# Performance work log

Measured on AMD Instinct MI355X. Metric: run time of the kernel, lower is better.

Reference implementation:

```python
import jax, jax.numpy as jnp
import numpy as np

SEQ, B, N, H, OUT, K, L = 32, 1024, 19, 128, 1, 2, 2


def setup_inputs() -> dict:
    key = jax.random.key(0)
    ks = jax.random.split(key, 16)
    s = lambda i, shape, scale=1.0: (jax.random.normal(ks[i], shape, jnp.float32) * scale)
    return {
        "inputs": s(0, (SEQ, B, N, OUT)),
        "initial_hidden_state": s(1, (L, B, N * H)),
        "support": s(2, (N, N)) * (1.0 / np.sqrt(N)),
        "W_gate0": s(3, (3 * (OUT + H), 2 * H)) * 0.05,
        "b_gate0": s(4, (2 * H,)) * 0.05,
        "W_cand0": s(5, (3 * (OUT + H), H)) * 0.05,
        "b_cand0": s(6, (H,)) * 0.05,
        "W_gate1": s(7, (3 * (H + H), 2 * H)) * 0.05,
        "b_gate1": s(8, (2 * H,)) * 0.05,
        "W_cand1": s(9, (3 * (H + H), H)) * 0.05,
        "b_cand1": s(10, (H,)) * 0.05,
        "W_proj": s(11, (H, OUT)) * 0.05,
        "b_proj": s(12, (OUT,)) * 0.05,
    }


def reference(inputs, initial_hidden_state, support, W_gate0, b_gate0, W_cand0,
              b_cand0, W_gate1, b_gate1, W_cand1, b_cand1, W_proj, b_proj):
    seq_len, batch = inputs.shape[0], inputs.shape[1]
    h0 = initial_hidden_state.reshape(L, batch, N, H)

    def gconv(x, W, b):
        # Chebyshev diffusion: x0, T1=S@x0, T2=2*S@T1-x0 (K=2, 1 support)
        x0 = x
        x1 = jnp.einsum('mn,bnf->bmf', support, x0)
        feats = [x0, x1]
        for _ in range(K - 1):
            x2 = 2.0 * jnp.einsum('mn,bnf->bmf', support, x1) - x0
            feats.append(x2)
            x0, x1 = x1, x2
        X = jnp.concatenate(feats, axis=-1)  # (B, N, F*num_matrices)
        return jnp.einsum('bnf,fo->bno', X, W) + b

    def cell(x_in, h, Wg, bg, Wc, bc):
        ru = jax.nn.sigmoid(gconv(jnp.concatenate([x_in, h], axis=-1), Wg, bg))
        r, u = jnp.split(ru, 2, axis=-1)
        c = jnp.tanh(gconv(jnp.concatenate([x_in, r * h], axis=-1), Wc, bc))
        return u * h + (1.0 - u) * c

    layer_params = [(W_gate0, b_gate0, W_cand0, b_cand0),
                    (W_gate1, b_gate1, W_cand1, b_cand1)]

    def step(carry, _):
        h, cur = carry
        new_h = []
        x = cur
        for i, (Wg, bg, Wc, bc) in enumerate(layer_params):
            x = cell(x, h[i], Wg, bg, Wc, bc)
            new_h.append(x)
        proj = jnp.einsum('bnh,ho->bno', x, W_proj) + b_proj  # (B, N, OUT)
        out_t = proj.reshape(batch, N * OUT)
        return (jnp.stack(new_h, axis=0), proj), out_t

    go = jnp.zeros((batch, N, OUT), inputs.dtype)
    (_, _), outputs = jax.lax.scan(step, (h0, go), None, length=seq_len)
    return outputs  # (seq_len, batch, N*OUT)
```

## Files before the change

kernel.cpp:

```cpp
#include <hip/hip_runtime.h>
#include <hip/hip_bf16.h>
#include <math.h>

#define SEQ   32
#define BATCH 1024
#define NN    19
#define HH    128
#define NB    4
#define MR    (NB*NN)
#define SAS   264
#define HS    132
#define UTS   72
#define NBLK  (BATCH/NB)
#define NT    512

#define OFF_G0 0
#define OFF_C0 122880
#define OFF_G1 184320
#define OFF_C1 380928
#define WTOT   479232

__device__ unsigned short g_wall[WTOT];
__device__ unsigned short g_tg[2048];

typedef __attribute__((ext_vector_type(8))) short  bf16x8;
typedef __attribute__((ext_vector_type(4))) float  f32x4;

__device__ __forceinline__ unsigned short f2bf(float v) {
    __hip_bfloat16 b = __float2bfloat16(v);
    return *reinterpret_cast<unsigned short*>(&b);
}
__device__ __forceinline__ float bf2f(unsigned short u) {
    unsigned int x = ((unsigned int)u) << 16;
    return __uint_as_float(x);
}
__device__ __forceinline__ float hload(const unsigned short* p) { return bf2f(*p); }
__device__ __forceinline__ float hload(const float* p)          { return *p; }
__device__ __forceinline__ void  hstore(unsigned short* p, float v) { *p = f2bf(v); }
__device__ __forceinline__ void  hstore(float* p, float v)          { *p = v; }

__global__ __launch_bounds__(256) void wconv_kernel(
    const float* __restrict__ W, int F, int O, int KP, int off)
{
    int idx = blockIdx.x*256 + threadIdx.x;
    int total = 3*O*KP;
    if (idx >= total) return;
    int j   = idx / (O*KP);
    int r   = idx - j*(O*KP);
    int col = r / KP;
    int k   = r - col*KP;
    float v = (k < F) ? W[(size_t)(j*F + k)*O + col] : 0.f;
    g_wall[off + idx] = f2bf(v);
}

__global__ __launch_bounds__(256) void tprime_kernel(const float* __restrict__ S)
{
    __shared__ float sS[NN*NN], sS2[NN*NN];
    int tid = threadIdx.x;
    for (int i = tid; i < NN*NN; i += 256) sS[i] = S[i];
    __syncthreads();
    for (int i = tid; i < NN*NN; i += 256) {
        int m = i/NN, n = i - m*NN;
        float a = 0.f;
        for (int k = 0; k < NN; ++k) a += sS[m*NN+k]*sS[k*NN+n];
        sS2[i] = a;
    }
    __syncthreads();
    for (int i = tid; i < 32*64; i += 256) {
        int m = i >> 6, k = i & 63;
        float v = 0.f;
        if (m < NN && k < 3*NN) {
            int j = k / NN, n = k - j*NN;
            float eye = (m == n) ? 1.f : 0.f;
            if (j == 0)      v = eye;
            else if (j == 1) v = sS[m*NN+n];
            else             v = 2.f*sS2[m*NN+n] - eye;
        }
        g_tg[i] = f2bf(v);
    }
}

#define LDS_BYTES 159664

template<int KS, int NTC, bool GATE, int XW, typename HT>
__device__ __forceinline__ void gconv_phase(
    const unsigned short* __restrict__ BT,
    const float* __restrict__ bias,
    HT* hL,
    unsigned short* sA,
    unsigned short* ub,
    unsigned short* UtW,
    int lane, int w)
{
    constexpr int OC = NTC*128;
    constexpr int KP = KS*32;
    const int r16 = lane & 15, quad = lane >> 4;
    const int sgo = w * (NTC*16);

    const unsigned short* wb[3][NTC];
    #pragma unroll
    for (int j = 0; j < 3; ++j)
        #pragma unroll
        for (int nt = 0; nt < NTC; ++nt)
            wb[j][nt] = BT + (size_t)(j*OC + sgo + nt*16 + r16)*KP + quad*8;

    f32x4 acc[3][5][NTC];
    #pragma unroll
    for (int j = 0; j < 3; ++j)
        #pragma unroll
        for (int mt = 0; mt < 5; ++mt)
            #pragma unroll
            for (int nt = 0; nt < NTC; ++nt) acc[j][mt][nt] = (f32x4)0.f;

    bf16x8 ring[2][3][NTC];
    #pragma unroll
    for (int j = 0; j < 3; ++j)
        #pragma unroll
        for (int nt = 0; nt < NTC; ++nt) {
            ring[0][j][nt] = *(const bf16x8*)(wb[j][nt]);
            if (KS > 1) ring[1][j][nt] = *(const bf16x8*)(wb[j][nt] + 32);
        }

    #pragma unroll
    for (int ks = 0; ks < KS; ++ks) {
        bf16x8 bcur[3][NTC];
        #pragma unroll
        for (int j = 0; j < 3; ++j)
            #pragma unroll
            for (int nt = 0; nt < NTC; ++nt) bcur[j][nt] = ring[ks & 1][j][nt];
        if (ks + 2 < KS) {
            #pragma unroll
            for (int j = 0; j < 3; ++j)
                #pragma unroll
                for (int nt = 0; nt < NTC; ++nt)
                    ring[ks & 1][j][nt] =
                        *(const bf16x8*)(wb[j][nt] + (ks + 2)*32);
        }
        #pragma unroll
        for (int mt = 0; mt < 5; ++mt) {
            bf16x8 af = *(const bf16x8*)&sA[(mt*16 + r16)*SAS + ks*32 + quad*8];
            #pragma unroll
            for (int j = 0; j < 3; ++j)
                #pragma unroll
                for (int nt = 0; nt < NTC; ++nt)
                    acc[j][mt][nt] = __builtin_amdgcn_mfma_f32_16x16x32_bf16(
                        af, bcur[j][nt], acc[j][mt][nt], 0, 0, 0);
        }
    }

    if (GATE) __syncthreads();

    float bv[NTC];
    #pragma unroll
    for (int nt = 0; nt < NTC; ++nt) bv[nt] = bias[sgo + nt*16 + r16];

    bf16x8 tp[2][2];
    #pragma unroll
    for (int mt2 = 0; mt2 < 2; ++mt2)
        #pragma unroll
        for (int kk = 0; kk < 2; ++kk)
            tp[mt2][kk] = *(const bf16x8*)&g_tg[(mt2*16 + r16)*64 + kk*32 + quad*8];

    for (int b = 0; b < NB; ++b) {
        #pragma unroll
        for (int j = 0; j < 3; ++j)
            #pragma unroll
            for (int mt = 0; mt < 5; ++mt)
                #pragma unroll
                for (int reg = 0; reg < 4; ++reg) {
                    int gm = mt*16 + quad*4 + reg;
                    int n  = gm - b*NN;
                    if (n >= 0 && n < NN) {
                        #pragma unroll
                        for (int nt = 0; nt < NTC; ++nt)
                            UtW[(nt*16 + r16)*UTS + j*NN + n] =
                                f2bf(acc[j][mt][nt][reg]);
                    }
                }
        f32x4 y[2][NTC];
        #pragma unroll
        for (int a = 0; a < 2; ++a)
            #pragma unroll
            for (int c = 0; c < NTC; ++c) y[a][c] = (f32x4)0.f;
        #pragma unroll
        for (int kk = 0; kk < 2; ++kk)
            #pragma unroll
            for (int nt = 0; nt < NTC; ++nt) {
                bf16x8 uf = *(const bf16x8*)&UtW[(nt*16 + r16)*UTS + kk*32 + quad*8];
                y[0][nt] = __builtin_amdgcn_mfma_f32_16x16x32_bf16(
                    tp[0][kk], uf, y[0][nt], 0, 0, 0);
                y[1][nt] = __builtin_amdgcn_mfma_f32_16x16x32_bf16(
                    tp[1][kk], uf, y[1][nt], 0, 0, 0);
            }
        #pragma unroll
        for (int mt2 = 0; mt2 < 2; ++mt2)
            #pragma unroll
            for (int nt = 0; nt < NTC; ++nt)
                #pragma unroll
                for (int reg = 0; reg < 4; ++reg) {
                    int m = mt2*16 + quad*4 + reg;
                    if (m < NN) {
                        int o = sgo + nt*16 + r16;
                        float v = y[mt2][nt][reg] + bv[nt];
                        int row = b*NN + m;
                        if (GATE) {
                            float sg_ = 1.f/(1.f + __expf(-v));
                            if (o < HH)
                                sA[row*SAS + XW + o] =
                                    f2bf(sg_ * hload(&hL[row*HS + o]));
                            else
                                ub[row*HS + (o-HH)] = f2bf(sg_);
                        } else {
                            float c  = 2.f/(1.f + __expf(-2.f*v)) - 1.f;
                            float u  = bf2f(ub[row*HS + o]);
                            float ho = hload(&hL[row*HS + o]);
                            hstore(&hL[row*HS + o], u*ho + (1.f - u)*c);
                        }
                    }
                }
    }
}

__global__ __launch_bounds__(NT, 2) void dcgru_persistent(
    const float* __restrict__ ihs,
    const float* __restrict__ bg0, const float* __restrict__ bc0,
    const float* __restrict__ bg1, const float* __restrict__ bc1,
    const float* __restrict__ Wp, const float* __restrict__ bp,
    float* __restrict__ out)
{
    extern __shared__ char smem[];
    unsigned short* h0    = (unsigned short*)smem;
    float*          h1    = (float*)(smem + 20064);
    unsigned short* sA    = (unsigned short*)(smem + 60192);
    unsigned short* ub    = (unsigned short*)(smem + 102432);
    unsigned short* Ut    = (unsigned short*)(smem + 122496);
    float*          xprev = (float*)(smem + 159360);

    const int tid  = threadIdx.x;
    const int lane = tid & 63;
    const int w    = tid >> 6;
    const int bb   = blockIdx.x * NB;
    unsigned short* UtW = Ut + w*32*UTS;

    const unsigned short* BTg0 = g_wall + OFF_G0;
    const unsigned short* BTc0 = g_wall + OFF_C0;
    const unsigned short* BTg1 = g_wall + OFF_G1;
    const unsigned short* BTc1 = g_wall + OFF_C1;

    for (int i = tid; i < MR*HH; i += NT) {
        int row = i >> 7, f = i & 127;
        h0[row*HS + f] = f2bf(ihs[(size_t)bb*2432 + i]);
        h1[row*HS + f] = ihs[(size_t)(BATCH + bb)*2432 + i];
    }
    for (int i = tid; i < MR; i += NT) xprev[i] = 0.f;
    for (int i = lane; i < 32*UTS; i += 64) UtW[i] = 0;

    const float wp0 = Wp[lane], wp1 = Wp[64 + lane], bpv = bp[0];
    __syncthreads();

    for (int t = 0; t < SEQ; ++t) {
        for (int idx = tid; idx < MR*160; idx += NT) {
            int row = idx/160, c = idx - row*160;
            unsigned short v;
            if (c == 0)       v = f2bf(xprev[row]);
            else if (c <= HH) v = h0[row*HS + (c-1)];
            else              v = 0;
            sA[row*SAS + c] = v;
        }
        __syncthreads();
        gconv_phase<5,2,true ,1>(BTg0, bg0, h0, sA, ub, UtW, lane, w);
        __syncthreads();
        gconv_phase<5,1,false,1>(BTc0, bc0, h0, sA, ub, UtW, lane, w);
        __syncthreads();

        for (int idx = tid; idx < MR*256; idx += NT) {
            int row = idx >> 8, c = idx & 255;
            sA[row*SAS + c] = (c < HH) ? h0[row*HS + c]
                                       : f2bf(h1[row*HS + (c-HH)]);
        }
        __syncthreads();
        gconv_phase<8,2,true ,HH>(BTg1, bg1, h1, sA, ub, UtW, lane, w);
        __syncthreads();
        gconv_phase<8,1,false,HH>(BTc1, bc1, h1, sA, ub, UtW, lane, w);
        __syncthreads();

        {
            int b  = w >> 1;
            int n0 = (w & 1) ? 10 : 0;
            int n1 = (w & 1) ? 19 : 10;
            for (int n = n0; n < n1; ++n) {
                int row = b*NN + n;
                float s = h1[row*HS + lane]*wp0 + h1[row*HS + 64 + lane]*wp1;
                #pragma unroll
                for (int off = 32; off; off >>= 1) s += __shfl_down(s, off, 64);
                if (lane == 0) {
                    float v = s + bpv;
                    out[((size_t)t*BATCH + bb + b)*NN + n] = v;
                    xprev[row] = v;
                }
            }
        }
        __syncthreads();
    }
}

extern "C" void kernel_launch(void* const* d_in, const int* in_sizes, int n_in,
                              void* d_out, int out_size, void* d_ws, size_t ws_size,
                              hipStream_t stream) {
    const float* ihs = (const float*)d_in[1];
    const float* S   = (const float*)d_in[2];
    const float* Wg0 = (const float*)d_in[3];
    const float* bg0 = (const float*)d_in[4];
    const float* Wc0 = (const float*)d_in[5];
    const float* bc0 = (const float*)d_in[6];
    const float* Wg1 = (const float*)d_in[7];
    const float* bg1 = (const float*)d_in[8];
    const float* Wc1 = (const float*)d_in[9];
    const float* bc1 = (const float*)d_in[10];
    const float* Wp  = (const float*)d_in[11];
    const float* bp  = (const float*)d_in[12];
    float* out = (float*)d_out;

    tprime_kernel<<<1, 256, 0, stream>>>(S);
    wconv_kernel<<<(3*256*160+255)/256, 256, 0, stream>>>(Wg0, 129, 256, 160, OFF_G0);
    wconv_kernel<<<(3*128*160+255)/256, 256, 0, stream>>>(Wc0, 129, 128, 160, OFF_C0);
    wconv_kernel<<<(3*256*256+255)/256, 256, 0, stream>>>(Wg1, 256, 256, 256, OFF_G1);
    wconv_kernel<<<(3*128*256+255)/256, 256, 0, stream>>>(Wc1, 256, 128, 256, OFF_C1);

    hipFuncSetAttribute((const void*)dcgru_persistent,
                        hipFuncAttributeMaxDynamicSharedMemorySize, LDS_BYTES);

    dcgru_persistent<<<NBLK, NT, LDS_BYTES, stream>>>(
        ihs, bg0, bc0, bg1, bc1, Wp, bp, out);
}
```

Measured before the change: 2.434 ms.

## Diffuse inputs before weight GEMM instead of diffusing per-weight outputs

Reorders the Chebyshev graph convolution so the support matrices (block-diagonal S and 2S²−I across the batch tile) are applied to the input features first via MFMA, and the three weight slices are then applied to X, S·X and T2·X in sequence. The old path used a per-batch U^T transpose through LDS and small diffusion MFMAs after the weight GEMM. The input column layout is also reordered (h first, x last) so that h0 can be copied with vectorised 16-byte loads. The cost is extra barriers between the three weight segments, ping-pong buffers A/B in LDS, and strided scalar LDS reads to build the diffusion operands.

```diff
diff --git a/kernel.cpp b/kernel.cpp
--- a/kernel.cpp
+++ b/kernel.cpp
@@ -9,8 +9,9 @@
 #define NB    4
 #define MR    (NB*NN)
 #define SAS   264
-#define HS    132
-#define UTS   72
+#define H0S   128
+#define H1S   132
+#define UBS   128
 #define NBLK  (BATCH/NB)
 #define NT    512
 
@@ -20,8 +21,16 @@
 #define OFF_C1 380928
 #define WTOT   479232
 
+#define OFF_H0 0
+#define OFF_H1 19456
+#define OFF_A  59584
+#define OFF_B  101824
+#define OFF_UB 144064
+#define OFF_XP 163520
+#define LDS_BYTES 163824
+
 __device__ unsigned short g_wall[WTOT];
-__device__ unsigned short g_tg[2048];
+__device__ unsigned short g_sb[2*80*96];
 
 typedef __attribute__((ext_vector_type(8))) short  bf16x8;
 typedef __attribute__((ext_vector_type(4))) float  f32x4;
@@ -40,7 +49,7 @@
 __device__ __forceinline__ void  hstore(float* p, float v)          { *p = v; }
 
 __global__ __launch_bounds__(256) void wconv_kernel(
-    const float* __restrict__ W, int F, int O, int KP, int off)
+    const float* __restrict__ W, int F, int O, int KP, int off, int l0)
 {
     int idx = blockIdx.x*256 + threadIdx.x;
     int total = 3*O*KP;
@@ -49,11 +58,14 @@
     int r   = idx - j*(O*KP);
     int col = r / KP;
     int k   = r - col*KP;
-    float v = (k < F) ? W[(size_t)(j*F + k)*O + col] : 0.f;
+    int src;
+    if (l0) src = (k < HH) ? k+1 : ((k == HH) ? 0 : -1);
+    else    src = (k < F) ? k : -1;
+    float v = (src >= 0) ? W[(size_t)(j*F + src)*O + col] : 0.f;
     g_wall[off + idx] = f2bf(v);
 }
 
-__global__ __launch_bounds__(256) void tprime_kernel(const float* __restrict__ S)
+__global__ __launch_bounds__(256) void sb_kernel(const float* __restrict__ S)
 {
     __shared__ float sS[NN*NN], sS2[NN*NN];
     int tid = threadIdx.x;
@@ -66,159 +78,178 @@
         sS2[i] = a;
     }
     __syncthreads();
-    for (int i = tid; i < 32*64; i += 256) {
-        int m = i >> 6, k = i & 63;
+    for (int i = tid; i < 2*80*96; i += 256) {
+        int mat = i / 7680;
+        int rr  = i - mat*7680;
+        int r   = rr / 96, k = rr - r*96;
         float v = 0.f;
-        if (m < NN && k < 3*NN) {
-            int j = k / NN, n = k - j*NN;
-            float eye = (m == n) ? 1.f : 0.f;
-            if (j == 0)      v = eye;
-            else if (j == 1) v = sS[m*NN+n];
-            else             v = 2.f*sS2[m*NN+n] - eye;
-        }
-        g_tg[i] = f2bf(v);
-    }
-}
-
-#define LDS_BYTES 159664
-
-template<int KS, int NTC, bool GATE, int XW, typename HT>
+        if (r < MR) {
+            int b = r / NN, m = r - b*NN;
+            int k0 = b*NN;
+            if (k >= k0 && k < k0 + NN) {
+                int n = k - k0;
+                v = (mat == 0) ? sS[m*NN+n]
+                               : (2.f*sS2[m*NN+n] - ((m==n)?1.f:0.f));
+            }
+        }
+        g_sb[i] = f2bf(v);
+    }
+}
+
+template<int KS, int NTC>
+__device__ __forceinline__ void load_wf(bf16x8 (&wf)[KS][NTC],
+    const unsigned short* __restrict__ Wj, int r16, int quad, int sgo)
+{
+    #pragma unroll
+    for (int ks = 0; ks < KS; ++ks)
+        #pragma unroll
+        for (int nt = 0; nt < NTC; ++nt)
+            wf[ks][nt] = *(const bf16x8*)(Wj +
+                (size_t)(sgo + nt*16 + r16)*(KS*32) + ks*32 + quad*8);
+}
+
+template<int KS, int NTC>
+__device__ __forceinline__ void mma_seg(f32x4 (&acc)[5][NTC],
+    const bf16x8 (&wf)[KS][NTC], const unsigned short* __restrict__ Ab,
+    int r16, int quad)
+{
+    #pragma unroll
+    for (int ks = 0; ks < KS; ++ks)
+        #pragma unroll
+        for (int mt = 0; mt < 5; ++mt) {
+            bf16x8 af = *(const bf16x8*)&Ab[(mt*16 + r16)*SAS + ks*32 + quad*8];
+            #pragma unroll
+            for (int nt = 0; nt < NTC; ++nt)
+                acc[mt][nt] = __builtin_amdgcn_mfma_f32_16x16x32_bf16(
+                    af, wf[ks][nt], acc[mt][nt], 0, 0, 0);
+        }
+}
+
+template<int KS, int NTC, bool GATE, int XW, int DCOLS, typename HT, int HSTR>
 __device__ __forceinline__ void gconv_phase(
-    const unsigned short* __restrict__ BT,
-    const float* __restrict__ bias,
-    HT* hL,
-    unsigned short* sA,
-    unsigned short* ub,
-    unsigned short* UtW,
+    const unsigned short* __restrict__ BT, const float* __restrict__ bias,
+    HT* __restrict__ hL,
+    unsigned short* __restrict__ Xb, unsigned short* __restrict__ Zb,
+    unsigned short* __restrict__ ub,
     int lane, int w)
 {
     constexpr int OC = NTC*128;
     constexpr int KP = KS*32;
     const int r16 = lane & 15, quad = lane >> 4;
-    const int sgo = w * (NTC*16);
-
-    const unsigned short* wb[3][NTC];
-    #pragma unroll
-    for (int j = 0; j < 3; ++j)
-        #pragma unroll
-        for (int nt = 0; nt < NTC; ++nt)
-            wb[j][nt] = BT + (size_t)(j*OC + sgo + nt*16 + r16)*KP + quad*8;
-
-    f32x4 acc[3][5][NTC];
-    #pragma unroll
-    for (int j = 0; j < 3; ++j)
+    const int sgo = w*(NTC*16);
+    const int c0  = w*32;
+    const bool dif = (c0 < DCOLS);
+
+    f32x4 z2a[5][2];
+    if (dif) {
+        constexpr int zmt[9] = {0,1,1,2,2,3,3,4,4};
+        constexpr int zks[9] = {0,0,1,0,1,1,2,1,2};
+        bf16x8 sb1[9], sb2[9], Bg[3][2];
+        #pragma unroll
+        for (int i = 0; i < 9; ++i) {
+            int o = (zmt[i]*16 + r16)*96 + zks[i]*32 + quad*8;
+            sb1[i] = *(const bf16x8*)&g_sb[o];
+            sb2[i] = *(const bf16x8*)&g_sb[7680 + o];
+        }
+        #pragma unroll
+        for (int kd = 0; kd < 3; ++kd)
+            #pragma unroll
+            for (int nt = 0; nt < 2; ++nt) {
+                bf16x8 v;
+                #pragma unroll
+                for (int e = 0; e < 8; ++e)
+                    v[e] = (short)Xb[(kd*32 + quad*8 + e)*SAS + c0 + nt*16 + r16];
+                Bg[kd][nt] = v;
+            }
+        f32x4 z1a[5][2];
         #pragma unroll
         for (int mt = 0; mt < 5; ++mt)
             #pragma unroll
-            for (int nt = 0; nt < NTC; ++nt) acc[j][mt][nt] = (f32x4)0.f;
-
-    bf16x8 ring[2][3][NTC];
-    #pragma unroll
-    for (int j = 0; j < 3; ++j)
-        #pragma unroll
-        for (int nt = 0; nt < NTC; ++nt) {
-            ring[0][j][nt] = *(const bf16x8*)(wb[j][nt]);
-            if (KS > 1) ring[1][j][nt] = *(const bf16x8*)(wb[j][nt] + 32);
-        }
-
-    #pragma unroll
-    for (int ks = 0; ks < KS; ++ks) {
-        bf16x8 bcur[3][NTC];
-        #pragma unroll
-        for (int j = 0; j < 3; ++j)
-            #pragma unroll
-            for (int nt = 0; nt < NTC; ++nt) bcur[j][nt] = ring[ks & 1][j][nt];
-        if (ks + 2 < KS) {
-            #pragma unroll
-            for (int j = 0; j < 3; ++j)
-                #pragma unroll
-                for (int nt = 0; nt < NTC; ++nt)
-                    ring[ks & 1][j][nt] =
-                        *(const bf16x8*)(wb[j][nt] + (ks + 2)*32);
-        }
-        #pragma unroll
-        for (int mt = 0; mt < 5; ++mt) {
-            bf16x8 af = *(const bf16x8*)&sA[(mt*16 + r16)*SAS + ks*32 + quad*8];
-            #pragma unroll
-            for (int j = 0; j < 3; ++j)
-                #pragma unroll
-                for (int nt = 0; nt < NTC; ++nt)
-                    acc[j][mt][nt] = __builtin_amdgcn_mfma_f32_16x16x32_bf16(
-                        af, bcur[j][nt], acc[j][mt][nt], 0, 0, 0);
-        }
-    }
-
-    if (GATE) __syncthreads();
+            for (int nt = 0; nt < 2; ++nt) {
+                z1a[mt][nt] = (f32x4)0.f; z2a[mt][nt] = (f32x4)0.f;
+            }
+        #pragma unroll
+        for (int i = 0; i < 9; ++i)
+            #pragma unroll
+            for (int nt = 0; nt < 2; ++nt) {
+                z1a[zmt[i]][nt] = __builtin_amdgcn_mfma_f32_16x16x32_bf16(
+                    sb1[i], Bg[zks[i]][nt], z1a[zmt[i]][nt], 0, 0, 0);
+                z2a[zmt[i]][nt] = __builtin_amdgcn_mfma_f32_16x16x32_bf16(
+                    sb2[i], Bg[zks[i]][nt], z2a[zmt[i]][nt], 0, 0, 0);
+            }
+        #pragma unroll
+        for (int mt = 0; mt < 5; ++mt)
+            #pragma unroll
+            for (int nt = 0; nt < 2; ++nt)
+                #pragma unroll
+                for (int reg = 0; reg < 4; ++reg)
+                    Zb[(mt*16 + quad*4 + reg)*SAS + c0 + nt*16 + r16] =
+                        f2bf(z1a[mt][nt][reg]);
+    }
+
+    f32x4 acc[5][NTC];
+    #pragma unroll
+    for (int mt = 0; mt < 5; ++mt)
+        #pragma unroll
+        for (int nt = 0; nt < NTC; ++nt) acc[mt][nt] = (f32x4)0.f;
+
+    {
+        bf16x8 wf[KS][NTC];
+        load_wf<KS,NTC>(wf, BT, r16, quad, sgo);
+        mma_seg<KS,NTC>(acc, wf, Xb, r16, quad);
+    }
+    __syncthreads();
+    if (dif) {
+        #pragma unroll
+        for (int mt = 0; mt < 5; ++mt)
+            #pragma unroll
+            for (int nt = 0; nt < 2; ++nt)
+                #pragma unroll
+                for (int reg = 0; reg < 4; ++reg)
+                    Xb[(mt*16 + quad*4 + reg)*SAS + c0 + nt*16 + r16] =
+                        f2bf(z2a[mt][nt][reg]);
+    }
+    {
+        bf16x8 wf[KS][NTC];
+        load_wf<KS,NTC>(wf, BT + (size_t)OC*KP, r16, quad, sgo);
+        mma_seg<KS,NTC>(acc, wf, Zb, r16, quad);
+    }
+    __syncthreads();
+    {
+        bf16x8 wf[KS][NTC];
+        load_wf<KS,NTC>(wf, BT + (size_t)2*OC*KP, r16, quad, sgo);
+        mma_seg<KS,NTC>(acc, wf, Xb, r16, quad);
+    }
 
     float bv[NTC];
     #pragma unroll
     for (int nt = 0; nt < NTC; ++nt) bv[nt] = bias[sgo + nt*16 + r16];
 
-    bf16x8 tp[2][2];
-    #pragma unroll
-    for (int mt2 = 0; mt2 < 2; ++mt2)
-        #pragma unroll
-        for (int kk = 0; kk < 2; ++kk)
-            tp[mt2][kk] = *(const bf16x8*)&g_tg[(mt2*16 + r16)*64 + kk*32 + quad*8];
-
-    for (int b = 0; b < NB; ++b) {
-        #pragma unroll
-        for (int j = 0; j < 3; ++j)
-            #pragma unroll
-            for (int mt = 0; mt < 5; ++mt)
-                #pragma unroll
-                for (int reg = 0; reg < 4; ++reg) {
-                    int gm = mt*16 + quad*4 + reg;
-                    int n  = gm - b*NN;
-                    if (n >= 0 && n < NN) {
-                        #pragma unroll
-                        for (int nt = 0; nt < NTC; ++nt)
-                            UtW[(nt*16 + r16)*UTS + j*NN + n] =
-                                f2bf(acc[j][mt][nt][reg]);
+    #pragma unroll
+    for (int mt = 0; mt < 5; ++mt)
+        #pragma unroll
+        for (int reg = 0; reg < 4; ++reg) {
+            int gm = mt*16 + quad*4 + reg;
+            if (gm < MR) {
+                #pragma unroll
+                for (int nt = 0; nt < NTC; ++nt) {
+                    int o = sgo + nt*16 + r16;
+                    float v = acc[mt][nt][reg] + bv[nt];
+                    if (GATE) {
+                        float sg_ = 1.f/(1.f + __expf(-v));
+                        if (o < HH)
+                            Zb[gm*SAS + XW + o] = f2bf(sg_ * hload(&hL[gm*HSTR + o]));
+                        else
+                            ub[gm*UBS + (o - HH)] = f2bf(sg_);
+                    } else {
+                        float c  = 2.f/(1.f + __expf(-2.f*v)) - 1.f;
+                        float u  = bf2f(ub[gm*UBS + o]);
+                        float ho = hload(&hL[gm*HSTR + o]);
+                        hstore(&hL[gm*HSTR + o], u*ho + (1.f - u)*c);
                     }
                 }
-        f32x4 y[2][NTC];
-        #pragma unroll
-        for (int a = 0; a < 2; ++a)
-            #pragma unroll
-            for (int c = 0; c < NTC; ++c) y[a][c] = (f32x4)0.f;
-        #pragma unroll
-        for (int kk = 0; kk < 2; ++kk)
-            #pragma unroll
-            for (int nt = 0; nt < NTC; ++nt) {
-                bf16x8 uf = *(const bf16x8*)&UtW[(nt*16 + r16)*UTS + kk*32 + quad*8];
-                y[0][nt] = __builtin_amdgcn_mfma_f32_16x16x32_bf16(
-                    tp[0][kk], uf, y[0][nt], 0, 0, 0);
-                y[1][nt] = __builtin_amdgcn_mfma_f32_16x16x32_bf16(
-                    tp[1][kk], uf, y[1][nt], 0, 0, 0);
-            }
-        #pragma unroll
-        for (int mt2 = 0; mt2 < 2; ++mt2)
-            #pragma unroll
-            for (int nt = 0; nt < NTC; ++nt)
-                #pragma unroll
-                for (int reg = 0; reg < 4; ++reg) {
-                    int m = mt2*16 + quad*4 + reg;
-                    if (m < NN) {
-                        int o = sgo + nt*16 + r16;
-                        float v = y[mt2][nt][reg] + bv[nt];
-                        int row = b*NN + m;
-                        if (GATE) {
-                            float sg_ = 1.f/(1.f + __expf(-v));
-                            if (o < HH)
-                                sA[row*SAS + XW + o] =
-                                    f2bf(sg_ * hload(&hL[row*HS + o]));
-                            else
-                                ub[row*HS + (o-HH)] = f2bf(sg_);
-                        } else {
-                            float c  = 2.f/(1.f + __expf(-2.f*v)) - 1.f;
-                            float u  = bf2f(ub[row*HS + o]);
-                            float ho = hload(&hL[row*HS + o]);
-                            hstore(&hL[row*HS + o], u*ho + (1.f - u)*c);
-                        }
-                    }
-                }
-    }
+            }
+        }
 }
 
 __global__ __launch_bounds__(NT, 2) void dcgru_persistent(
@@ -229,18 +260,17 @@
     float* __restrict__ out)
 {
     extern __shared__ char smem[];
-    unsigned short* h0    = (unsigned short*)smem;
-    float*          h1    = (float*)(smem + 20064);
-    unsigned short* sA    = (unsigned short*)(smem + 60192);
-    unsigned short* ub    = (unsigned short*)(smem + 102432);
-    unsigned short* Ut    = (unsigned short*)(smem + 122496);
-    float*          xprev = (float*)(smem + 159360);
+    unsigned short* h0 = (unsigned short*)(smem + OFF_H0);
+    float*          h1 = (float*)(smem + OFF_H1);
+    unsigned short* A  = (unsigned short*)(smem + OFF_A);
+    unsigned short* Bb = (unsigned short*)(smem + OFF_B);
+    unsigned short* ub = (unsigned short*)(smem + OFF_UB);
+    float*       xprev = (float*)(smem + OFF_XP);
 
     const int tid  = threadIdx.x;
     const int lane = tid & 63;
     const int w    = tid >> 6;
     const int bb   = blockIdx.x * NB;
-    unsigned short* UtW = Ut + w*32*UTS;
 
     const unsigned short* BTg0 = g_wall + OFF_G0;
     const unsigned short* BTc0 = g_wall + OFF_C0;
@@ -248,40 +278,60 @@
     const unsigned short* BTc1 = g_wall + OFF_C1;
 
     for (int i = tid; i < MR*HH; i += NT) {
-        int row = i >> 7, f = i & 127;
-        h0[row*HS + f] = f2bf(ihs[(size_t)bb*2432 + i]);
-        h1[row*HS + f] = ihs[(size_t)(BATCH + bb)*2432 + i];
+        h0[i] = f2bf(ihs[(size_t)bb*2432 + i]);
+        h1[(i >> 7)*H1S + (i & 127)] = ihs[(size_t)(BATCH + bb)*2432 + i];
     }
     for (int i = tid; i < MR; i += NT) xprev[i] = 0.f;
-    for (int i = lane; i < 32*UTS; i += 64) UtW[i] = 0;
-
+    for (int i = tid; i < 80*SAS/8; i += NT) {
+        ((bf16x8*)A)[i]  = (bf16x8)(short)0;
+        ((bf16x8*)Bb)[i] = (bf16x8)(short)0;
+    }
     const float wp0 = Wp[lane], wp1 = Wp[64 + lane], bpv = bp[0];
     __syncthreads();
 
     for (int t = 0; t < SEQ; ++t) {
-        for (int idx = tid; idx < MR*160; idx += NT) {
-            int row = idx/160, c = idx - row*160;
-            unsigned short v;
-            if (c == 0)       v = f2bf(xprev[row]);
-            else if (c <= HH) v = h0[row*HS + (c-1)];
-            else              v = 0;
-            sA[row*SAS + c] = v;
-        }
-        __syncthreads();
-        gconv_phase<5,2,true ,1>(BTg0, bg0, h0, sA, ub, UtW, lane, w);
-        __syncthreads();
-        gconv_phase<5,1,false,1>(BTc0, bc0, h0, sA, ub, UtW, lane, w);
-        __syncthreads();
-
-        for (int idx = tid; idx < MR*256; idx += NT) {
-            int row = idx >> 8, c = idx & 255;
-            sA[row*SAS + c] = (c < HH) ? h0[row*HS + c]
-                                       : f2bf(h1[row*HS + (c-HH)]);
-        }
-        __syncthreads();
-        gconv_phase<8,2,true ,HH>(BTg1, bg1, h1, sA, ub, UtW, lane, w);
-        __syncthreads();
-        gconv_phase<8,1,false,HH>(BTc1, bc1, h1, sA, ub, UtW, lane, w);
+        for (int i = tid; i < MR*16; i += NT) {
+            int row = i >> 4, ch = i & 15;
+            *(bf16x8*)&A[row*SAS + ch*8] =
+                *(const bf16x8*)&h0[row*H0S + ch*8];
+        }
+        for (int i = tid; i < MR*32; i += NT) {
+            int row = i >> 5, c = i & 31;
+            A[row*SAS + HH + c] = (c == 0) ? f2bf(xprev[row]) : (unsigned short)0;
+        }
+        __syncthreads();
+        gconv_phase<5,2,true ,0,160,unsigned short,H0S>(BTg0, bg0, h0, A, Bb, ub, lane, w);
+        for (int i = tid; i < MR; i += NT) Bb[i*SAS + HH] = f2bf(xprev[i]);
+        __syncthreads();
+        gconv_phase<5,1,false,0,160,unsigned short,H0S>(BTc0, bc0, h0, Bb, A, ub, lane, w);
+        __syncthreads();
+
+        for (int i = tid; i < MR*16; i += NT) {
+            int row = i >> 4, ch = i & 15;
+            *(bf16x8*)&A[row*SAS + ch*8] =
+                *(const bf16x8*)&h0[row*H0S + ch*8];
+        }
+        for (int i = tid; i < MR*16; i += NT) {
+            int row = i >> 4, ch = i & 15;
+            const float* hp = &h1[row*H1S + ch*8];
+            f32x4 x0 = *(const f32x4*)hp;
+            f32x4 x1 = *(const f32x4*)(hp + 4);
+            bf16x8 v;
+            v[0] = (short)f2bf(x0[0]); v[1] = (short)f2bf(x0[1]);
+            v[2] = (short)f2bf(x0[2]); v[3] = (short)f2bf(x0[3]);
+            v[4] = (short)f2bf(x1[0]); v[5] = (short)f2bf(x1[1]);
+            v[6] = (short)f2bf(x1[2]); v[7] = (short)f2bf(x1[3]);
+            *(bf16x8*)&A[row*SAS + HH + ch*8] = v;
+        }
+        __syncthreads();
+        gconv_phase<8,2,true ,HH,256,float,H1S>(BTg1, bg1, h1, A, Bb, ub, lane, w);
+        for (int i = tid; i < MR*16; i += NT) {
+            int row = i >> 4, ch = i & 15;
+            *(bf16x8*)&Bb[row*SAS + ch*8] =
+                *(const bf16x8*)&h0[row*H0S + ch*8];
+        }
+        __syncthreads();
+        gconv_phase<8,1,false,HH,256,float,H1S>(BTc1, bc1, h1, Bb, A, ub, lane, w);
         __syncthreads();
 
         {
@@ -290,7 +340,7 @@
             int n1 = (w & 1) ? 19 : 10;
             for (int n = n0; n < n1; ++n) {
                 int row = b*NN + n;
-                float s = h1[row*HS + lane]*wp0 + h1[row*HS + 64 + lane]*wp1;
+                float s = h1[row*H1S + lane]*wp0 + h1[row*H1S + 64 + lane]*wp1;
                 #pragma unroll
                 for (int off = 32; off; off >>= 1) s += __shfl_down(s, off, 64);
                 if (lane == 0) {
@@ -321,11 +371,11 @@
     const float* bp  = (const float*)d_in[12];
     float* out = (float*)d_out;
 
-    tprime_kernel<<<1, 256, 0, stream>>>(S);
-    wconv_kernel<<<(3*256*160+255)/256, 256, 0, stream>>>(Wg0, 129, 256, 160, OFF_G0);
-    wconv_kernel<<<(3*128*160+255)/256, 256, 0, stream>>>(Wc0, 129, 128, 160, OFF_C0);
-    wconv_kernel<<<(3*256*256+255)/256, 256, 0, stream>>>(Wg1, 256, 256, 256, OFF_G1);
-    wconv_kernel<<<(3*128*256+255)/256, 256, 0, stream>>>(Wc1, 256, 128, 256, OFF_C1);
+    sb_kernel<<<1, 256, 0, stream>>>(S);
+    wconv_kernel<<<(3*256*160+255)/256, 256, 0, stream>>>(Wg0, 129, 256, 160, OFF_G0, 1);
+    wconv_kernel<<<(3*128*160+255)/256, 256, 0, stream>>>(Wc0, 129, 128, 160, OFF_C0, 1);
+    wconv_kernel<<<(3*256*256+255)/256, 256, 0, stream>>>(Wg1, 256, 256, 256, OFF_G1, 0);
+    wconv_kernel<<<(3*128*256+255)/256, 256, 0, stream>>>(Wc1, 256, 128, 256, OFF_C1, 0);
 
     hipFuncSetAttribute((const void*)dcgru_persistent,
                         hipFuncAttributeMaxDynamicSharedMemorySize, LDS_BYTES);
```

After: 3.963 ms. 62.8% more time.
